# Kernel tuning notes

Hardware: AMD Instinct MI355X
Metric: run time of the kernel (lower is better)

## Reference

```python
import jax, jax.numpy as jnp
import numpy as np

NUM_VARS = 22
LAYERS = 2
N = 2 ** NUM_VARS


def setup_inputs() -> dict:
    key = jax.random.key(0)
    k1, k2, k3, k4 = jax.random.split(key, 4)
    h = jax.random.normal(k1, (N,), dtype=jnp.float32)          # unsatisfied-clause 'energy' per bitstring
    hS = jax.random.uniform(k2, (N,), dtype=jnp.float32)        # satisfiability weight per bitstring
    gamma = jax.random.normal(k3, (LAYERS,), dtype=jnp.float32) * 0.01
    beta = jax.random.normal(k4, (LAYERS,), dtype=jnp.float32) * 0.01
    return {"h": h, "hS": hS, "gamma": gamma, "beta": beta}


def reference(h, hS, gamma, beta):
    n = NUM_VARS
    # |+>^n initial state: uniform amplitudes 1/sqrt(N)
    circuit = jnp.full((N,), 1.0 / np.sqrt(N), dtype=jnp.complex64)
    for l in range(LAYERS):
        # cost unitary: elementwise phase exp(i * gamma * h)
        circuit = jnp.exp((1j * gamma[l] * h).astype(jnp.complex64)) * circuit
        # mixing unitary: per-qubit X-rotation butterfly.
        # torch's transpose(0,i)+split+cat swaps the two slices along qubit axis i,
        # which for a size-2 axis is exactly a flip along that axis.
        cb = jnp.cos(beta[l]).astype(jnp.complex64)
        sb = (1j * jnp.sin(beta[l])).astype(jnp.complex64)
        c = circuit.reshape((2,) * n)
        for i in range(n):  # fixed small loop over qubits (structurally distinct axes)
            c = cb * c + sb * jnp.flip(c, axis=i)
        circuit = c.reshape(N)
    ps = jnp.real(circuit * jnp.conj(circuit))  # |amplitude|^2
    return jnp.dot(ps, hS)
```

## Files before the change

### kernel.cpp

```cpp
#include <hip/hip_runtime.h>


#define NTOT    (1u << 22)
#define LO_BITS 13
#define HI_BITS 9
#define LO      (1u << LO_BITS)
#define HI      (1u << HI_BITS)
#define GRP     32
#define TPB     512
#define TPB2    1024
#define R       16

typedef __fp16 h2_t __attribute__((ext_vector_type(2)));
union PkU { unsigned u; h2_t h; };

__device__ __forceinline__ unsigned pk(float x, float y) {
    PkU p; p.h = __builtin_amdgcn_cvt_pkrtz(x, y); return p.u;
}
__device__ __forceinline__ float2 unpk(unsigned v) {
    PkU p; p.u = v; return make_float2((float)p.h.x, (float)p.h.y);
}

#define REGSTAGE(MASK, CB, SB) {                                  \
    _Pragma("unroll")                                             \
    for (int r0 = 0; r0 < R; ++r0) {                              \
        if ((r0 & (MASK)) == 0) {                                 \
            const int r1 = r0 | (MASK);                           \
            float t0r = re[r0], t0i = im[r0];                     \
            float t1r = re[r1], t1i = im[r1];                     \
            re[r0] = (CB) * t0r - (SB) * t1i;                     \
            im[r0] = (CB) * t0i + (SB) * t1r;                     \
            re[r1] = (CB) * t1r - (SB) * t0i;                     \
            im[r1] = (CB) * t1i + (SB) * t0r;                     \
        } } }

#define SHFLSTAGE(MASK, CB, SB) {                                 \
    _Pragma("unroll")                                             \
    for (int r = 0; r < R; ++r) {                                 \
        unsigned pv = (unsigned)__shfl_xor((int)pk(re[r], im[r]), (MASK), 64); \
        float2 p = unpk(pv);                                      \
        float tr = re[r], ti = im[r];                             \
        re[r] = (CB) * tr - (SB) * p.y;                           \
        im[r] = (CB) * ti + (SB) * p.x;                           \
    } }

__global__ __launch_bounds__(TPB, 4) void k_init_low(
    const float* __restrict__ h, const float* __restrict__ gam,
    const float* __restrict__ bet, unsigned* __restrict__ st,
    float* __restrict__ out)
{
    __shared__ unsigned sC[LO];
    const float g1 = gam[0];
    const float cb = __cosf(bet[0]), sb = __sinf(bet[0]);
    const unsigned t = threadIdx.x, lane = t & 63u, wave = t >> 6;
    const size_t base = (size_t)blockIdx.x * LO;
    float re[R], im[R];

    if (blockIdx.x == 0 && t == 0) out[0] = 0.f;

    #pragma unroll
    for (int r = 0; r < R; ++r) {
        float s, c;
        __sincosf(g1 * h[base + (unsigned)r * TPB + t], &s, &c);
        re[r] = c * 0x1p-11f;
        im[r] = s * 0x1p-11f;
    }
    REGSTAGE(1, cb, sb)  REGSTAGE(2, cb, sb)
    REGSTAGE(4, cb, sb)  REGSTAGE(8, cb, sb)
    SHFLSTAGE(1,  cb, sb) SHFLSTAGE(2,  cb, sb)
    SHFLSTAGE(4,  cb, sb) SHFLSTAGE(8,  cb, sb)
    SHFLSTAGE(16, cb, sb) SHFLSTAGE(32, cb, sb)
    #pragma unroll
    for (int r = 0; r < R; ++r) sC[(unsigned)r * TPB + t] = pk(re[r], im[r]);
    __syncthreads();
    #pragma unroll
    for (int r = 0; r < R; ++r) {
        unsigned j = lane | ((unsigned)(r & 7) << 6) | (wave << 9) | ((unsigned)(r >> 3) << 12);
        float2 v = unpk(sC[j]); re[r] = v.x; im[r] = v.y;
    }
    REGSTAGE(1, cb, sb)  REGSTAGE(2, cb, sb)  REGSTAGE(4, cb, sb)
    #pragma unroll
    for (int r = 0; r < R; ++r) {
        unsigned j = lane | ((unsigned)(r & 7) << 6) | (wave << 9) | ((unsigned)(r >> 3) << 12);
        st[base + j] = pk(re[r], im[r]);
    }
}

__global__ __launch_bounds__(TPB2, 4) void k_high(
    const float* __restrict__ h, const float* __restrict__ gam,
    const float* __restrict__ bet, unsigned* __restrict__ st)
{
    __shared__ unsigned sC[GRP * HI];
    const float g2  = gam[1];
    const float cb1 = __cosf(bet[0]), sb1 = __sinf(bet[0]);
    const float cb2 = __cosf(bet[1]), sb2 = __sinf(bet[1]);
    const unsigned t = threadIdx.x, lane = t & 63u, w = t >> 6;
    const unsigned g  = lane & 31u;
    const unsigned h0 = lane >> 5;
    const unsigned lo0 = blockIdx.x * GRP;
    float re[R], im[R];

    #pragma unroll
    for (int r = 0; r < R; ++r) {
        unsigned hi = h0 | (w << 1) | ((unsigned)r << 5);
        float2 v = unpk(st[(size_t)hi * LO + lo0 + g]);
        re[r] = v.x; im[r] = v.y;
    }
    REGSTAGE(1, cb1, sb1)  REGSTAGE(2, cb1, sb1)
    REGSTAGE(4, cb1, sb1)  REGSTAGE(8, cb1, sb1)
    SHFLSTAGE(32, cb1, sb1)
    #pragma unroll
    for (int r = 0; r < R; ++r)
        sC[g | (h0 << 5) | (w << 6) | ((unsigned)r << 10)] = pk(re[r], im[r]);
    __syncthreads();
    #pragma unroll
    for (int r = 0; r < R; ++r) {
        float2 v = unpk(sC[g | (h0 << 5) | ((unsigned)r << 6) | (w << 10)]);
        re[r] = v.x; im[r] = v.y;
    }
    REGSTAGE(1, cb1, sb1)  REGSTAGE(2, cb1, sb1)
    REGSTAGE(4, cb1, sb1)  REGSTAGE(8, cb1, sb1)
    #pragma unroll
    for (int r = 0; r < R; ++r) {
        unsigned hi = h0 | ((unsigned)r << 1) | (w << 5);
        float s, c;
        __sincosf(g2 * h[(size_t)hi * LO + lo0 + g], &s, &c);
        float tr = re[r], ti = im[r];
        re[r] = tr * c - ti * s;
        im[r] = tr * s + ti * c;
    }
    REGSTAGE(1, cb2, sb2)  REGSTAGE(2, cb2, sb2)
    REGSTAGE(4, cb2, sb2)  REGSTAGE(8, cb2, sb2)
    SHFLSTAGE(32, cb2, sb2)
    __syncthreads();
    #pragma unroll
    for (int r = 0; r < R; ++r)
        sC[g | (h0 << 5) | ((unsigned)r << 6) | (w << 10)] = pk(re[r], im[r]);
    __syncthreads();
    #pragma unroll
    for (int r = 0; r < R; ++r) {
        float2 v = unpk(sC[g | (h0 << 5) | (w << 6) | ((unsigned)r << 10)]);
        re[r] = v.x; im[r] = v.y;
    }
    REGSTAGE(1, cb2, sb2)  REGSTAGE(2, cb2, sb2)
    REGSTAGE(4, cb2, sb2)  REGSTAGE(8, cb2, sb2)
    #pragma unroll
    for (int r = 0; r < R; ++r) {
        unsigned hi = h0 | (w << 1) | ((unsigned)r << 5);
        st[(size_t)hi * LO + lo0 + g] = pk(re[r], im[r]);
    }
}

__global__ __launch_bounds__(TPB, 4) void k_low2(
    const float* __restrict__ hS, const float* __restrict__ bet,
    const unsigned* __restrict__ st, float* __restrict__ out)
{
    __shared__ unsigned sC[LO];
    __shared__ float wsum[TPB / 64];
    const float cb = __cosf(bet[1]), sb = __sinf(bet[1]);
    const unsigned t = threadIdx.x, lane = t & 63u, wave = t >> 6;
    const size_t base = (size_t)blockIdx.x * LO;
    float re[R], im[R];

    #pragma unroll
    for (int r = 0; r < R; ++r) {
        float2 v = unpk(st[base + (unsigned)r * TPB + t]);
        re[r] = v.x; im[r] = v.y;
    }
    REGSTAGE(1, cb, sb)  REGSTAGE(2, cb, sb)
    REGSTAGE(4, cb, sb)  REGSTAGE(8, cb, sb)
    SHFLSTAGE(1,  cb, sb) SHFLSTAGE(2,  cb, sb)
    SHFLSTAGE(4,  cb, sb) SHFLSTAGE(8,  cb, sb)
    SHFLSTAGE(16, cb, sb) SHFLSTAGE(32, cb, sb)
    #pragma unroll
    for (int r = 0; r < R; ++r) sC[(unsigned)r * TPB + t] = pk(re[r], im[r]);
    __syncthreads();
    #pragma unroll
    for (int r = 0; r < R; ++r) {
        unsigned j = lane | ((unsigned)(r & 7) << 6) | (wave << 9) | ((unsigned)(r >> 3) << 12);
        float2 v = unpk(sC[j]); re[r] = v.x; im[r] = v.y;
    }
    REGSTAGE(1, cb, sb)  REGSTAGE(2, cb, sb)  REGSTAGE(4, cb, sb)
    float acc = 0.f;
    #pragma unroll
    for (int r = 0; r < R; ++r) {
        unsigned j = lane | ((unsigned)(r & 7) << 6) | (wave << 9) | ((unsigned)(r >> 3) << 12);
        acc = fmaf(re[r] * re[r] + im[r] * im[r], hS[base + j], acc);
    }
    #pragma unroll
    for (int off = 32; off >= 1; off >>= 1)
        acc += __shfl_down(acc, off, 64);
    if (lane == 0) wsum[wave] = acc;
    __syncthreads();
    if (t == 0) {
        float s = 0.f;
        #pragma unroll
        for (int w = 0; w < TPB / 64; ++w) s += wsum[w];
        unsafeAtomicAdd(out, s);
    }
}

extern "C" void kernel_launch(void* const* d_in, const int* in_sizes, int n_in,
                              void* d_out, int out_size, void* d_ws, size_t ws_size,
                              hipStream_t stream)
{
    (void)in_sizes; (void)n_in; (void)out_size; (void)ws_size;
    const float* h   = (const float*)d_in[0];
    const float* hS  = (const float*)d_in[1];
    const float* gam = (const float*)d_in[2];
    const float* bet = (const float*)d_in[3];
    unsigned* st = (unsigned*)d_ws;
    float* out   = (float*)d_out;

    k_init_low<<<dim3(NTOT / LO), dim3(TPB),  0, stream>>>(h, gam, bet, st, out);
    k_high    <<<dim3(LO / GRP),  dim3(TPB2), 0, stream>>>(h, gam, bet, st);
    k_low2    <<<dim3(NTOT / LO), dim3(TPB),  0, stream>>>(hS, bet, st, out);
}
```

Measured before the change: 120.9 us.

## Use 1024-thread blocks with 8 regs/thread and fp32 shared staging in low kernels

```diff
diff --git a/kernel.cpp b/kernel.cpp
--- a/kernel.cpp
+++ b/kernel.cpp
@@ -7,8 +7,9 @@
 #define LO      (1u << LO_BITS)
 #define HI      (1u << HI_BITS)
 #define GRP     32
-#define TPB     512
+#define TPB1    1024
 #define TPB2    1024
+#define R8      8
 #define R       16
 
 typedef __fp16 h2_t __attribute__((ext_vector_type(2)));
@@ -21,9 +22,9 @@
     PkU p; p.u = v; return make_float2((float)p.h.x, (float)p.h.y);
 }
 
-#define REGSTAGE(MASK, CB, SB) {                                  \
+#define REGSTAGE_N(NR, MASK, CB, SB) {                            \
     _Pragma("unroll")                                             \
-    for (int r0 = 0; r0 < R; ++r0) {                              \
+    for (int r0 = 0; r0 < (NR); ++r0) {                           \
         if ((r0 & (MASK)) == 0) {                                 \
             const int r1 = r0 | (MASK);                           \
             float t0r = re[r0], t0i = im[r0];                     \
@@ -34,6 +35,16 @@
             im[r1] = (CB) * t1i + (SB) * t0r;                     \
         } } }
 
+#define SHFLSTAGE_N(NR, MASK, CB, SB) {                           \
+    _Pragma("unroll")                                             \
+    for (int r = 0; r < (NR); ++r) {                              \
+        float tr = re[r], ti = im[r];                             \
+        float pr = __shfl_xor(tr, (MASK), 64);                    \
+        float pi = __shfl_xor(ti, (MASK), 64);                    \
+        re[r] = (CB) * tr - (SB) * pi;                            \
+        im[r] = (CB) * ti + (SB) * pr;                            \
+    } }
+
 #define SHFLSTAGE(MASK, CB, SB) {                                 \
     _Pragma("unroll")                                             \
     for (int r = 0; r < R; ++r) {                                 \
@@ -43,45 +54,56 @@
         re[r] = (CB) * tr - (SB) * p.y;                           \
         im[r] = (CB) * ti + (SB) * p.x;                           \
     } }
-
-__global__ __launch_bounds__(TPB, 4) void k_init_low(
+#define REGSTAGE(MASK, CB, SB) REGSTAGE_N(R, MASK, CB, SB)
+
+__global__ __launch_bounds__(TPB1, 8) void k_init_low(
     const float* __restrict__ h, const float* __restrict__ gam,
     const float* __restrict__ bet, unsigned* __restrict__ st,
     float* __restrict__ out)
 {
-    __shared__ unsigned sC[LO];
+    __shared__ float2 sC[LO];
     const float g1 = gam[0];
     const float cb = __cosf(bet[0]), sb = __sinf(bet[0]);
-    const unsigned t = threadIdx.x, lane = t & 63u, wave = t >> 6;
+    const unsigned t = threadIdx.x, lane = t & 63u, w = t >> 6;
     const size_t base = (size_t)blockIdx.x * LO;
-    float re[R], im[R];
+    float re[R8], im[R8];
 
     if (blockIdx.x == 0 && t == 0) out[0] = 0.f;
 
     #pragma unroll
-    for (int r = 0; r < R; ++r) {
+    for (int r = 0; r < R8; ++r) {
         float s, c;
-        __sincosf(g1 * h[base + (unsigned)r * TPB + t], &s, &c);
+        __sincosf(g1 * h[base + (unsigned)r * TPB1 + t], &s, &c);
         re[r] = c * 0x1p-11f;
         im[r] = s * 0x1p-11f;
     }
-    REGSTAGE(1, cb, sb)  REGSTAGE(2, cb, sb)
-    REGSTAGE(4, cb, sb)  REGSTAGE(8, cb, sb)
-    SHFLSTAGE(1,  cb, sb) SHFLSTAGE(2,  cb, sb)
-    SHFLSTAGE(4,  cb, sb) SHFLSTAGE(8,  cb, sb)
-    SHFLSTAGE(16, cb, sb) SHFLSTAGE(32, cb, sb)
-    #pragma unroll
-    for (int r = 0; r < R; ++r) sC[(unsigned)r * TPB + t] = pk(re[r], im[r]);
-    __syncthreads();
-    #pragma unroll
-    for (int r = 0; r < R; ++r) {
-        unsigned j = lane | ((unsigned)(r & 7) << 6) | (wave << 9) | ((unsigned)(r >> 3) << 12);
-        float2 v = unpk(sC[j]); re[r] = v.x; im[r] = v.y;
-    }
-    REGSTAGE(1, cb, sb)  REGSTAGE(2, cb, sb)  REGSTAGE(4, cb, sb)
-    #pragma unroll
-    for (int r = 0; r < R; ++r) {
-        unsigned j = lane | ((unsigned)(r & 7) << 6) | (wave << 9) | ((unsigned)(r >> 3) << 12);
+    REGSTAGE_N(R8, 1, cb, sb)  REGSTAGE_N(R8, 2, cb, sb)  REGSTAGE_N(R8, 4, cb, sb)
+    SHFLSTAGE_N(R8, 1,  cb, sb) SHFLSTAGE_N(R8, 2,  cb, sb)
+    SHFLSTAGE_N(R8, 4,  cb, sb) SHFLSTAGE_N(R8, 8,  cb, sb)
+    SHFLSTAGE_N(R8, 16, cb, sb) SHFLSTAGE_N(R8, 32, cb, sb)
+    #pragma unroll
+    for (int r = 0; r < R8; ++r) sC[(unsigned)r * TPB1 + t] = make_float2(re[r], im[r]);
+    __syncthreads();
+    #pragma unroll
+    for (int r = 0; r < R8; ++r) {
+        unsigned j = lane | ((unsigned)r << 6) | ((w & 8u) << 6) | ((w & 7u) << 10);
+        float2 v = sC[j]; re[r] = v.x; im[r] = v.y;
+    }
+    REGSTAGE_N(R8, 1, cb, sb)  REGSTAGE_N(R8, 2, cb, sb)  REGSTAGE_N(R8, 4, cb, sb)
+    __syncthreads();
+    #pragma unroll
+    for (int r = 0; r < R8; ++r) {
+        unsigned j = lane | ((unsigned)r << 6) | ((w & 8u) << 6) | ((w & 7u) << 10);
+        sC[j] = make_float2(re[r], im[r]);
+    }
+    __syncthreads();
+    #pragma unroll
+    for (int r = 0; r < R8; ++r) {
+        unsigned j = lane | ((unsigned)r << 6) | ((w & 8u) << 6) | ((w & 7u) << 10);
+        float2 p = sC[j ^ 512u];
+        float tr = re[r], ti = im[r];
+        re[r] = cb * tr - sb * p.y;
+        im[r] = cb * ti + sb * p.x;
         st[base + j] = pk(re[r], im[r]);
     }
 }
@@ -151,51 +173,60 @@
     }
 }
 
-__global__ __launch_bounds__(TPB, 4) void k_low2(
+__global__ __launch_bounds__(TPB1, 8) void k_low2(
     const float* __restrict__ hS, const float* __restrict__ bet,
     const unsigned* __restrict__ st, float* __restrict__ out)
 {
-    __shared__ unsigned sC[LO];
-    __shared__ float wsum[TPB / 64];
+    __shared__ float2 sC[LO];
+    __shared__ float wsum[TPB1 / 64];
     const float cb = __cosf(bet[1]), sb = __sinf(bet[1]);
-    const unsigned t = threadIdx.x, lane = t & 63u, wave = t >> 6;
+    const unsigned t = threadIdx.x, lane = t & 63u, w = t >> 6;
     const size_t base = (size_t)blockIdx.x * LO;
-    float re[R], im[R];
-
-    #pragma unroll
-    for (int r = 0; r < R; ++r) {
-        float2 v = unpk(st[base + (unsigned)r * TPB + t]);
-        re[r] = v.x; im[r] = v.y;
-    }
-    REGSTAGE(1, cb, sb)  REGSTAGE(2, cb, sb)
-    REGSTAGE(4, cb, sb)  REGSTAGE(8, cb, sb)
-    SHFLSTAGE(1,  cb, sb) SHFLSTAGE(2,  cb, sb)
-    SHFLSTAGE(4,  cb, sb) SHFLSTAGE(8,  cb, sb)
-    SHFLSTAGE(16, cb, sb) SHFLSTAGE(32, cb, sb)
-    #pragma unroll
-    for (int r = 0; r < R; ++r) sC[(unsigned)r * TPB + t] = pk(re[r], im[r]);
-    __syncthreads();
-    #pragma unroll
-    for (int r = 0; r < R; ++r) {
-        unsigned j = lane | ((unsigned)(r & 7) << 6) | (wave << 9) | ((unsigned)(r >> 3) << 12);
-        float2 v = unpk(sC[j]); re[r] = v.x; im[r] = v.y;
-    }
-    REGSTAGE(1, cb, sb)  REGSTAGE(2, cb, sb)  REGSTAGE(4, cb, sb)
+    float re[R8], im[R8];
+
+    #pragma unroll
+    for (int r = 0; r < R8; ++r) {
+        float2 v = unpk(st[base + (unsigned)r * TPB1 + t]);
+        re[r] = v.x; im[r] = v.y;
+    }
+    REGSTAGE_N(R8, 1, cb, sb)  REGSTAGE_N(R8, 2, cb, sb)  REGSTAGE_N(R8, 4, cb, sb)
+    SHFLSTAGE_N(R8, 1,  cb, sb) SHFLSTAGE_N(R8, 2,  cb, sb)
+    SHFLSTAGE_N(R8, 4,  cb, sb) SHFLSTAGE_N(R8, 8,  cb, sb)
+    SHFLSTAGE_N(R8, 16, cb, sb) SHFLSTAGE_N(R8, 32, cb, sb)
+    #pragma unroll
+    for (int r = 0; r < R8; ++r) sC[(unsigned)r * TPB1 + t] = make_float2(re[r], im[r]);
+    __syncthreads();
+    #pragma unroll
+    for (int r = 0; r < R8; ++r) {
+        unsigned j = lane | ((unsigned)r << 6) | ((w & 8u) << 6) | ((w & 7u) << 10);
+        float2 v = sC[j]; re[r] = v.x; im[r] = v.y;
+    }
+    REGSTAGE_N(R8, 1, cb, sb)  REGSTAGE_N(R8, 2, cb, sb)  REGSTAGE_N(R8, 4, cb, sb)
+    __syncthreads();
+    #pragma unroll
+    for (int r = 0; r < R8; ++r) {
+        unsigned j = lane | ((unsigned)r << 6) | ((w & 8u) << 6) | ((w & 7u) << 10);
+        sC[j] = make_float2(re[r], im[r]);
+    }
+    __syncthreads();
     float acc = 0.f;
     #pragma unroll
-    for (int r = 0; r < R; ++r) {
-        unsigned j = lane | ((unsigned)(r & 7) << 6) | (wave << 9) | ((unsigned)(r >> 3) << 12);
-        acc = fmaf(re[r] * re[r] + im[r] * im[r], hS[base + j], acc);
+    for (int r = 0; r < R8; ++r) {
+        unsigned j = lane | ((unsigned)r << 6) | ((w & 8u) << 6) | ((w & 7u) << 10);
+        float2 p = sC[j ^ 512u];
+        float tr = cb * re[r] - sb * p.y;
+        float ti = cb * im[r] + sb * p.x;
+        acc = fmaf(tr * tr + ti * ti, hS[base + j], acc);
     }
     #pragma unroll
     for (int off = 32; off >= 1; off >>= 1)
         acc += __shfl_down(acc, off, 64);
-    if (lane == 0) wsum[wave] = acc;
+    if (lane == 0) wsum[w] = acc;
     __syncthreads();
     if (t == 0) {
         float s = 0.f;
         #pragma unroll
-        for (int w = 0; w < TPB / 64; ++w) s += wsum[w];
+        for (int i = 0; i < TPB1 / 64; ++i) s += wsum[i];
         unsafeAtomicAdd(out, s);
     }
 }
@@ -212,7 +243,7 @@
     unsigned* st = (unsigned*)d_ws;
     float* out   = (float*)d_out;
 
-    k_init_low<<<dim3(NTOT / LO), dim3(TPB),  0, stream>>>(h, gam, bet, st, out);
+    k_init_low<<<dim3(NTOT / LO), dim3(TPB1), 0, stream>>>(h, gam, bet, st, out);
     k_high    <<<dim3(LO / GRP),  dim3(TPB2), 0, stream>>>(h, gam, bet, st);
-    k_low2    <<<dim3(NTOT / LO), dim3(TPB),  0, stream>>>(hS, bet, st, out);
-}
+    k_low2    <<<dim3(NTOT / LO), dim3(TPB1), 0, stream>>>(hS, bet, st, out);
+}
```

Result: slower. 127.7 us (+5.7%).
